# Optimization experiments

Hardware: AMD Instinct MI355X
Metric: run time of the kernel (lower is better)

Reference implementation:

```python
import jax, jax.numpy as jnp
import numpy as np
import math

WS = 8      # window_size
SS = 4      # stride = window_size // 2
NHEADS = 4

def _grid(size, ws, ss):
    n = (size - ws) // ss + 1
    return jnp.arange(n)[:, None] * ss + jnp.arange(ws)[None, :]  # (n, ws)

def _unfold(x, ws, ss):
    # x: (B,C,Hp,Wp) -> (B, L, C, ws*ws), matching torch F.unfold ordering
    B, C, Hp, Wp = x.shape
    ri = _grid(Hp, ws, ss)
    ci = _grid(Wp, ws, ss)
    p = x[:, :, ri][:, :, :, :, ci]  # (B,C,nH,ws,nW,ws)
    nH, nW = ri.shape[0], ci.shape[0]
    p = p.transpose(0, 2, 4, 1, 3, 5).reshape(B, nH * nW, C, ws * ws)
    return p, nH, nW

def _fold(p, Hp, Wp, nH, nW, ws, ss):
    # p: (B, L, C, ws*ws) -> overlap-add to (B,C,Hp,Wp), matching torch F.fold
    B, L, C, _ = p.shape
    p = p.reshape(B, nH, nW, C, ws, ws).transpose(0, 3, 1, 4, 2, 5)  # (B,C,nH,ws,nW,ws)
    rr = _grid(Hp, ws, ss)[:, :, None, None]   # (nH,ws,1,1)
    cc = _grid(Wp, ws, ss)[None, None, :, :]   # (1,1,nW,ws)
    return jnp.zeros((B, C, Hp, Wp), p.dtype).at[:, :, rr, cc].add(p)

def _se(h, w1, w2):
    # squeeze-excite: global avg pool -> 1x1 reduce -> relu -> 1x1 expand -> sigmoid gate
    pooled = h.mean(axis=(2, 3))                                # (B, gc)
    s = jax.nn.sigmoid(jax.nn.relu(pooled @ w1.T) @ w2.T)       # (B, gc)
    return h * s[:, :, None, None]

def _forward(low, high, w_ql, w_kh, w_vh, w_qh, w_kl, w_vl, w_proj_l, w_proj_h,
             se0_w1, se0_w2, se1_w1, se1_w2, se2_w1, se2_w2):
    B, C, H, W = low.shape
    ws, ss = WS, SS
    n_h = 0 if H <= ws else math.ceil((H - ws) / ss)
    n_w = 0 if W <= ws else math.ceil((W - ws) / ss)
    Hp, Wp = n_h * ss + ws, n_w * ss + ws
    pad = ((0, 0), (0, 0), (0, Hp - H), (0, Wp - W))
    low_p = jnp.pad(low, pad)
    high_p = jnp.pad(high, pad)
    base, rem = divmod(C, 3)
    chs = [base + (1 if i < rem else 0) for i in range(3)]
    ofs = np.cumsum([0] + chs)
    sew = [(se0_w1, se0_w2), (se1_w1, se1_w2), (se2_w1, se2_w2)]
    high_dir = jnp.concatenate(
        [_se(high_p[:, ofs[i]:ofs[i + 1]], *sew[i]) for i in range(3)], axis=1)
    lw, nH, nW = _unfold(low_p, ws, ss)    # (B,L,C,Np)
    hw, _, _ = _unfold(high_dir, ws, ss)
    L, Np, d = lw.shape[1], ws * ws, C // NHEADS
    scale = d ** -0.5
    proj = lambda x, w: jnp.einsum('oc,blcn->blon', w, x).reshape(B, L, NHEADS, d, Np)
    a_lh = jax.nn.softmax(jnp.einsum('blhdn,blhdm->blhnm', proj(lw, w_ql), proj(hw, w_kh)) * scale, axis=-1)
    a_hl = jax.nn.softmax(jnp.einsum('blhdn,blhdm->blhnm', proj(hw, w_qh), proj(lw, w_kl)) * scale, axis=-1)
    ol = jnp.einsum('blhnm,blhdm->blhdn', a_lh, proj(hw, w_vh)).reshape(B, L, C, Np)
    oh = jnp.einsum('blhnm,blhdm->blhdn', a_hl, proj(lw, w_vl)).reshape(B, L, C, Np)
    mask = _fold(jnp.ones((1, L, 1, Np), low.dtype), Hp, Wp, nH, nW, ws, ss)  # overlap counts
    out_l = (_fold(ol, Hp, Wp, nH, nW, ws, ss) / mask)[:, :, :H, :W]
    out_h = (_fold(oh, Hp, Wp, nH, nW, ws, ss) / mask)[:, :, :H, :W]
    return (low + jnp.einsum('oc,bchw->bohw', w_proj_l, out_l),
            high + jnp.einsum('oc,bchw->bohw', w_proj_h, out_h))

def setup_inputs() -> dict:
    key = jax.random.key(0)
    ks = jax.random.split(key, 20)
    B, C, H, W = 4, 64, 128, 128
    chs = [22, 21, 21]
    d = {
        'low': jax.random.normal(ks[0], (B, C, H, W), jnp.float32),
        'high': jax.random.normal(ks[1], (B, C, H, W), jnp.float32),
    }
    for i, n in enumerate(['w_ql', 'w_kh', 'w_vh', 'w_qh', 'w_kl', 'w_vl', 'w_proj_l', 'w_proj_h']):
        d[n] = jax.random.normal(ks[2 + i], (C, C), jnp.float32) * (C ** -0.5)
    for i, gc in enumerate(chs):
        d[f'se{i}_w1'] = jax.random.normal(ks[10 + 2 * i], (1, gc), jnp.float32) * 0.1
        d[f'se{i}_w2'] = jax.random.normal(ks[11 + 2 * i], (gc, 1), jnp.float32) * 0.1
    return d

def reference(low, high, w_ql, w_kh, w_vh, w_qh, w_kl, w_vl, w_proj_l, w_proj_h,
              se0_w1, se0_w2, se1_w1, se1_w2, se2_w1, se2_w2):
    return _forward(low, high, w_ql, w_kh, w_vh, w_qh, w_kl, w_vl, w_proj_l, w_proj_h,
                    se0_w1, se0_w2, se1_w1, se1_w2, se2_w1, se2_w2)
```

## Files before the change

### kernel.cpp

```cpp
#include <hip/hip_runtime.h>

typedef short short8 __attribute__((ext_vector_type(8)));
typedef short short4v __attribute__((ext_vector_type(4)));
typedef float f4 __attribute__((ext_vector_type(4)));

#define NB 4
#define NHW 128
#define NPX (NHW*NHW)
#define NWIN 31
#define NL (NWIN*NWIN)
#define SWV(r,c) (((r)<<6) + (((((c)>>3) ^ ((r)&7))<<3) | ((c)&7)))
#define MFMA(a,b,c) __builtin_amdgcn_mfma_f32_16x16x32_bf16(a,b,c,0,0,0)

__device__ __forceinline__ short f2bf(float f) {
    unsigned u = __float_as_uint(f);
    u += 0x7fffu + ((u >> 16) & 1u);
    return (short)(u >> 16);
}
__device__ __forceinline__ float bf2f(short v) {
    return __uint_as_float(((unsigned)(unsigned short)v) << 16);
}

__global__ void k_pool(const float* __restrict__ high, float* __restrict__ pooled) {
    int bc = blockIdx.x;
    const float* src = high + (size_t)bc * NPX;
    float s = 0.f;
    for (int i = threadIdx.x; i < NPX; i += 256) s += src[i];
    for (int off = 32; off > 0; off >>= 1) s += __shfl_down(s, off);
    __shared__ float red[4];
    int lane = threadIdx.x & 63, wv = threadIdx.x >> 6;
    if (lane == 0) red[wv] = s;
    __syncthreads();
    if (threadIdx.x == 0)
        pooled[bc] = (red[0] + red[1] + red[2] + red[3]) * (1.f / NPX);
}

__global__ void k_gate(const float* __restrict__ pooled,
                       const float* __restrict__ w10, const float* __restrict__ w20,
                       const float* __restrict__ w11, const float* __restrict__ w21,
                       const float* __restrict__ w12, const float* __restrict__ w22,
                       float* __restrict__ sgate) {
    __shared__ float pl[256];
    int t = threadIdx.x;
    pl[t] = pooled[t];
    __syncthreads();
    int b = t >> 6, c = t & 63;
    const float* w1; const float* w2; int o0, gc;
    if (c < 22)      { w1 = w10; w2 = w20; o0 = 0;  gc = 22; }
    else if (c < 43) { w1 = w11; w2 = w21; o0 = 22; gc = 21; }
    else             { w1 = w12; w2 = w22; o0 = 43; gc = 21; }
    float a = 0.f;
    for (int k = 0; k < gc; ++k) a += pl[b*64 + o0 + k] * w1[k];
    a = fmaxf(a, 0.f);
    float z = a * w2[c - o0];
    sgate[t] = 1.f / (1.f + __expf(-z));
}

__device__ __forceinline__ void wrange(int x, int& lo, int& hi) {
    lo = (x >= 7) ? ((x - 4) >> 2) : 0;
    hi = x >> 2; if (hi > 30) hi = 30;
}

template<int EMIT>
__global__ __launch_bounds__(256, 6) void k_proj(
    const float* __restrict__ src, const float* __restrict__ gate,
    const float* __restrict__ Wq, const float* __restrict__ Wk, const float* __restrict__ Wv,
    short* __restrict__ Qp, short* __restrict__ Kp, short* __restrict__ Vp) {
    __shared__ __align__(16) short T[8192];
    int b = blockIdx.x >> 7, row = blockIdx.x & 127;
    int t = threadIdx.x;
    const float* sp = src + (size_t)b*64*NPX + row*NHW;
    #pragma unroll
    for (int i = 0; i < 8; ++i) {
        int f = t + i*256;
        int c = f & 63, px = (f >> 6) << 2;
        float4 v = *(const float4*)(sp + (size_t)c*NPX + px);
        float g = gate ? gate[b*64 + c] : 1.f;
        T[SWV(px + 0, c)] = f2bf(v.x * g);
        T[SWV(px + 1, c)] = f2bf(v.y * g);
        T[SWV(px + 2, c)] = f2bf(v.z * g);
        T[SWV(px + 3, c)] = f2bf(v.w * g);
    }
    __syncthreads();
    int w = t >> 6, ln = t & 63, l16 = ln & 15, quad = ln >> 4;
    int orow = 16*w + l16;
    short8 wq[2], wk[2], wv[2];
    #pragma unroll
    for (int kf = 0; kf < 2; ++kf) {
        if (EMIT & 1) {
            const float* p = Wq + orow*64 + kf*32 + quad*8;
            #pragma unroll
            for (int j = 0; j < 8; ++j) wq[kf][j] = f2bf(p[j]);
        }
        if (EMIT & 2) {
            const float* p = Wk + orow*64 + kf*32 + quad*8;
            #pragma unroll
            for (int j = 0; j < 8; ++j) wk[kf][j] = f2bf(p[j]);
        }
        if (EMIT & 4) {
            const float* p = Wv + orow*64 + kf*32 + quad*8;
            #pragma unroll
            for (int j = 0; j < 8; ++j) wv[kf][j] = f2bf(p[j]);
        }
    }
    #pragma unroll
    for (int nt = 0; nt < 8; ++nt) {
        int px = nt*16 + l16;
        short8 xb0 = *(const short8*)(T + SWV(px, quad*8));
        short8 xb1 = *(const short8*)(T + SWV(px, 32 + quad*8));
        size_t clbase = ((size_t)b*NPX + row*NHW + px)*64 + 16*w + quad*4;
        if (EMIT & 1) {
            f4 acc = {0.f,0.f,0.f,0.f};
            acc = MFMA(wq[0], xb0, acc); acc = MFMA(wq[1], xb1, acc);
            short4v sv;
            #pragma unroll
            for (int r = 0; r < 4; ++r) sv[r] = f2bf(acc[r]);
            *(short4v*)(Qp + clbase) = sv;
        }
        if (EMIT & 2) {
            f4 acc = {0.f,0.f,0.f,0.f};
            acc = MFMA(wk[0], xb0, acc); acc = MFMA(wk[1], xb1, acc);
            short4v sv;
            #pragma unroll
            for (int r = 0; r < 4; ++r) sv[r] = f2bf(acc[r]);
            *(short4v*)(Kp + clbase) = sv;
        }
        if (EMIT & 4) {
            f4 acc = {0.f,0.f,0.f,0.f};
            acc = MFMA(wv[0], xb0, acc); acc = MFMA(wv[1], xb1, acc);
            #pragma unroll
            for (int r = 0; r < 4; ++r)
                Vp[((size_t)(b*64 + 16*w + quad*4 + r))*NPX + row*NHW + px] = f2bf(acc[r]);
        }
    }
}

template<int SWZ>
__global__ __launch_bounds__(256, 6) void k_attn(
    const short* __restrict__ Q0, const short* __restrict__ K0, const short* __restrict__ V0,
    const short* __restrict__ Q1, const short* __restrict__ K1, const short* __restrict__ V1,
    short* __restrict__ scr, size_t scr_stride, int nb) {
    __shared__ __align__(16) short Pb[4][1024];
    int bidx = blockIdx.x;
    int pass, b, l;
    if (SWZ) {
        int region = bidx & 7;
        pass = region >> 2; b = region & 3; l = bidx >> 3;
    } else {
        int per = nb * NL;
        pass = bidx / per; int rem2 = bidx - pass*per;
        b = rem2 / NL; l = rem2 - b*NL;
    }
    const short* Qp = pass ? Q1 : Q0;
    const short* Kp = pass ? K1 : K0;
    const short* Vp = pass ? V1 : V0;
    short* scrp = scr + (size_t)pass * scr_stride;
    int wr = l / NWIN, wc = l - (l/NWIN)*NWIN;
    int row0 = wr*4, col0 = wc*4;
    int parity = (wr & 1)*2 + (wc & 1);
    int t = threadIdx.x, w = t >> 6, ln = t & 63, l16 = ln & 15, quad = ln >> 4;
    int h = w;
    short* PT = Pb[w];
    short8 z = {0,0,0,0,0,0,0,0};

    short8 kb[4];
    #pragma unroll
    for (int mt = 0; mt < 4; ++mt) {
        int m = mt*16 + l16;
        int px = (row0 + (m >> 3))*NHW + col0 + (m & 7);
        kb[mt] = (quad < 2) ? *(const short8*)(Kp + ((size_t)b*NPX + px)*64 + h*16 + quad*8) : z;
    }
    short8 va0, va1;
    {
        const short* vb = Vp + ((size_t)(b*64 + h*16 + l16))*NPX;
        const short* p0 = vb + (row0 + quad)*NHW + col0;
        const short* p1 = vb + (row0 + 4 + quad)*NHW + col0;
        short4v a = *(const short4v*)p0, bq = *(const short4v*)(p0 + 4);
        short4v c = *(const short4v*)p1, d = *(const short4v*)(p1 + 4);
        #pragma unroll
        for (int j = 0; j < 4; ++j) { va0[j] = a[j]; va0[4+j] = bq[j]; va1[j] = c[j]; va1[4+j] = d[j]; }
    }

    #pragma unroll
    for (int ntl = 0; ntl < 4; ++ntl) {
        int n = ntl*16 + l16;
        int px = (row0 + (n >> 3))*NHW + col0 + (n & 7);
        short8 qa = (quad < 2) ? *(const short8*)(Qp + ((size_t)b*NPX + px)*64 + h*16 + quad*8) : z;
        f4 s[4];
        #pragma unroll
        for (int mt = 0; mt < 4; ++mt) {
            f4 acc = {0.f,0.f,0.f,0.f};
            s[mt] = MFMA(qa, kb[mt], acc);
        }
        f4 sum = {0.f,0.f,0.f,0.f};
        #pragma unroll
        for (int mt = 0; mt < 4; ++mt)
            #pragma unroll
            for (int r = 0; r < 4; ++r) {
                float e = __expf(fminf(s[mt][r]*0.25f, 30.f));
                s[mt][r] = e; sum[r] += e;
            }
        #pragma unroll
        for (int d = 1; d < 16; d <<= 1)
            #pragma unroll
            for (int r = 0; r < 4; ++r) sum[r] += __shfl_xor(sum[r], d);
        #pragma unroll
        for (int r = 0; r < 4; ++r) sum[r] = 1.f / sum[r];
        #pragma unroll
        for (int mt = 0; mt < 4; ++mt)
            #pragma unroll
            for (int r = 0; r < 4; ++r)
                PT[SWV(quad*4 + r, mt*16 + l16)] = f2bf(s[mt][r] * sum[r]);
        f4 o = {0.f,0.f,0.f,0.f};
        o = MFMA(va0, *(const short8*)(PT + SWV(l16, quad*8)), o);
        o = MFMA(va1, *(const short8*)(PT + SWV(l16, 32 + quad*8)), o);
        short4v sv;
        #pragma unroll
        for (int r = 0; r < 4; ++r) sv[r] = f2bf(o[r]);
        *(short4v*)(scrp + (((size_t)(parity*nb + b))*NPX + px)*64 + h*16 + quad*4) = sv;
    }
}

__global__ __launch_bounds__(256, 6) void k_gather(
    const short* __restrict__ scr, size_t scr_stride,
    const float* __restrict__ r0, const float* __restrict__ r1,
    const float* __restrict__ wp0, const float* __restrict__ wp1,
    float* __restrict__ o0, float* __restrict__ o1, int nb) {
    __shared__ __align__(16) short G[8192];
    int bidx = blockIdx.x;
    int per = nb * NHW;
    int pass = bidx / per; int rem2 = bidx - pass*per;
    int b = rem2 >> 7, hh = rem2 & 127;
    const short* scrp = scr + (size_t)pass * scr_stride;
    const float* resid = pass ? r1 : r0;
    const float* wproj = pass ? wp1 : wp0;
    float* outp = pass ? o1 : o0;
    int t = threadIdx.x;
    int p = t >> 1, c0 = (t & 1)*32;
    int rlo, rhi, clo, chi;
    wrange(hh, rlo, rhi); wrange(p, clo, chi);
    float vr[2], vc[2];
    vr[0] = (rhi > rlo || (rlo & 1) == 0) ? 1.f : 0.f;
    vr[1] = (rhi > rlo || (rlo & 1) == 1) ? 1.f : 0.f;
    vc[0] = (chi > clo || (clo & 1) == 0) ? 1.f : 0.f;
    vc[1] = (chi > clo || (clo & 1) == 1) ? 1.f : 0.f;
    float g[32];
    #pragma unroll
    for (int k = 0; k < 32; ++k) g[k] = 0.f;
    #pragma unroll
    for (int par = 0; par < 4; ++par) {
        float wgt = vr[par >> 1] * vc[par & 1];
        const short* srcp = scrp + (((size_t)(par*nb + b))*NPX + hh*NHW + p)*64 + c0;
        #pragma unroll
        for (int k4 = 0; k4 < 4; ++k4) {
            short8 v = *(const short8*)(srcp + k4*8);
            #pragma unroll
            for (int j = 0; j < 8; ++j) g[k4*8 + j] += wgt * bf2f(v[j]);
        }
    }
    float inv = 1.f / ((float)(rhi - rlo + 1) * (float)(chi - clo + 1));
    #pragma unroll
    for (int k4 = 0; k4 < 4; ++k4) {
        short8 v;
        #pragma unroll
        for (int j = 0; j < 8; ++j) v[j] = f2bf(g[k4*8 + j] * inv);
        *(short8*)(G + SWV(p, c0 + k4*8)) = v;
    }
    __syncthreads();
    int w = t >> 6, ln = t & 63, l16 = ln & 15, quad = ln >> 4;
    short8 wa0, wa1;
    {
        const float* p0 = wproj + (16*w + l16)*64 + quad*8;
        #pragma unroll
        for (int j = 0; j < 8; ++j) { wa0[j] = f2bf(p0[j]); wa1[j] = f2bf(p0[32 + j]); }
    }
    #pragma unroll
    for (int pt = 0; pt < 8; ++pt) {
        f4 acc = {0.f,0.f,0.f,0.f};
        acc = MFMA(wa0, *(const short8*)(G + SWV(pt*16 + l16, quad*8)), acc);
        acc = MFMA(wa1, *(const short8*)(G + SWV(pt*16 + l16, 32 + quad*8)), acc);
        #pragma unroll
        for (int r = 0; r < 4; ++r) {
            size_t gi = (((size_t)(b*64 + 16*w + quad*4 + r))*NHW + hh)*NHW + pt*16 + l16;
            outp[gi] = resid[gi] + acc[r];
        }
    }
}

extern "C" void kernel_launch(void* const* d_in, const int* in_sizes, int n_in,
                              void* d_out, int out_size, void* d_ws, size_t ws_size,
                              hipStream_t stream) {
    const float* low  = (const float*)d_in[0];
    const float* high = (const float*)d_in[1];
    const float* w_ql = (const float*)d_in[2];
    const float* w_kh = (const float*)d_in[3];
    const float* w_vh = (const float*)d_in[4];
    const float* w_qh = (const float*)d_in[5];
    const float* w_kl = (const float*)d_in[6];
    const float* w_vl = (const float*)d_in[7];
    const float* w_pl = (const float*)d_in[8];
    const float* w_ph = (const float*)d_in[9];
    float* out = (float*)d_out;
    float* pooled = (float*)d_ws;
    float* sgate  = pooled + 256;
    short* base = (short*)((char*)d_ws + 2048);
    const size_t PL = (size_t)NB * NPX * 64;
    const size_t plane_f = (size_t)NB * 64 * NPX;
    const size_t SCR = 4 * PL;
    size_t need_fused  = 2048 + (6*PL + 2*SCR) * sizeof(short);
    size_t need_serial = 2048 + (6*PL + SCR) * sizeof(short);
    size_t scr_elems_per_b = 4 * (size_t)NPX * 64;

    k_pool<<<dim3(NB*64), dim3(256), 0, stream>>>(high, pooled);
    k_gate<<<dim3(1), dim3(256), 0, stream>>>(pooled,
        (const float*)d_in[10], (const float*)d_in[11],
        (const float*)d_in[12], (const float*)d_in[13],
        (const float*)d_in[14], (const float*)d_in[15], sgate);

    if (ws_size >= need_serial) {
        short* QL = base;        short* KL = base + PL;   short* VL = base + 2*PL;
        short* QH = base + 3*PL; short* KH = base + 4*PL; short* VH = base + 5*PL;
        short* scr = base + 6*PL;
        k_proj<7><<<dim3(NB*NHW), dim3(256), 0, stream>>>(low,  nullptr, w_ql, w_kl, w_vl, QL, KL, VL);
        k_proj<7><<<dim3(NB*NHW), dim3(256), 0, stream>>>(high, sgate,   w_qh, w_kh, w_vh, QH, KH, VH);
        if (ws_size >= need_fused) {
            k_attn<1><<<dim3(8*NL), dim3(256), 0, stream>>>(QL, KH, VH, QH, KL, VL, scr, SCR, NB);
            k_gather<<<dim3(2*NB*NHW), dim3(256), 0, stream>>>(scr, SCR, low, high,
                w_pl, w_ph, out, out + plane_f, NB);
        } else {
            k_attn<0><<<dim3(NB*NL), dim3(256), 0, stream>>>(QL, KH, VH, nullptr, nullptr, nullptr, scr, 0, NB);
            k_gather<<<dim3(NB*NHW), dim3(256), 0, stream>>>(scr, 0, low, nullptr,
                w_pl, nullptr, out, nullptr, NB);
            k_attn<0><<<dim3(NB*NL), dim3(256), 0, stream>>>(QH, KL, VL, nullptr, nullptr, nullptr, scr, 0, NB);
            k_gather<<<dim3(NB*NHW), dim3(256), 0, stream>>>(scr, 0, high, nullptr,
                w_ph, nullptr, out + plane_f, nullptr, NB);
        }
    } else {
        short* P0 = base; short* P1 = base + PL; short* P2 = base + 2*PL;
        short* scr = base + 3*PL;
        int nbc = 0;
        for (int n = NB; n >= 1; n >>= 1)
            if (ws_size >= 2048 + (3*PL + n*scr_elems_per_b)*sizeof(short)) { nbc = n; break; }
        if (nbc == 0) nbc = 1;
        for (int pass = 0; pass < 2; ++pass) {
            const float* qsrc = pass ? high : low;
            const float* ksrc = pass ? low  : high;
            const float* qg   = pass ? sgate : nullptr;
            const float* kg   = pass ? nullptr : sgate;
            const float* Wq   = pass ? w_qh : w_ql;
            const float* Wk   = pass ? w_kl : w_kh;
            const float* Wv   = pass ? w_vl : w_vh;
            const float* Wp   = pass ? w_ph : w_pl;
            const float* resid = pass ? high : low;
            float* op = out + (size_t)pass * plane_f;
            k_proj<1><<<dim3(NB*NHW), dim3(256), 0, stream>>>(qsrc, qg, Wq, nullptr, nullptr, P0, nullptr, nullptr);
            k_proj<6><<<dim3(NB*NHW), dim3(256), 0, stream>>>(ksrc, kg, nullptr, Wk, Wv, nullptr, P1, P2);
            for (int b0 = 0; b0 < NB; b0 += nbc) {
                int nb = (NB - b0) < nbc ? (NB - b0) : nbc;
                size_t boff = (size_t)b0 * NPX * 64;
                k_attn<0><<<dim3(nb*NL), dim3(256), 0, stream>>>(P0 + boff, P1 + boff, P2 + boff,
                    nullptr, nullptr, nullptr, scr, 0, nb);
                k_gather<<<dim3(nb*NHW), dim3(256), 0, stream>>>(scr, 0, resid + boff, nullptr,
                    Wp, nullptr, op + boff, nullptr, nb);
            }
        }
    }
}
```

Measured before the change: 246.6 us.

## Merge projection launches, compute softmax denominator via MFMA, split gather blocks

The two projection launches become one kernel that picks low or high source by block region, and the 0.25 score scale is folded into Q at projection time. In attention, the shuffle-based softmax sum is replaced by a ones-vector MFMA over the truncated-bf16 probabilities, with normalisation applied after the PV product. Gather blocks now cover half a row each, with the grid doubled and pass/batch interleaved. The goals are to cut launch overhead, cross-lane reductions and per-block register/LDS use, at the cost of bf16 truncation error in the unnormalised probabilities.

After: 218.3 us. 11.5% less time.

```diff
diff --git a/kernel.cpp b/kernel.cpp
--- a/kernel.cpp
+++ b/kernel.cpp
@@ -16,6 +16,9 @@
     unsigned u = __float_as_uint(f);
     u += 0x7fffu + ((u >> 16) & 1u);
     return (short)(u >> 16);
+}
+__device__ __forceinline__ short f2bft(float f) {
+    return (short)(__float_as_uint(f) >> 16);
 }
 __device__ __forceinline__ float bf2f(short v) {
     return __uint_as_float(((unsigned)(unsigned short)v) << 16);
@@ -62,13 +65,11 @@
 }
 
 template<int EMIT>
-__global__ __launch_bounds__(256, 6) void k_proj(
+__device__ __forceinline__ void proj_body(
     const float* __restrict__ src, const float* __restrict__ gate,
     const float* __restrict__ Wq, const float* __restrict__ Wk, const float* __restrict__ Wv,
-    short* __restrict__ Qp, short* __restrict__ Kp, short* __restrict__ Vp) {
-    __shared__ __align__(16) short T[8192];
-    int b = blockIdx.x >> 7, row = blockIdx.x & 127;
-    int t = threadIdx.x;
+    short* __restrict__ Qp, short* __restrict__ Kp, short* __restrict__ Vp,
+    short* T, int b, int row, int t) {
     const float* sp = src + (size_t)b*64*NPX + row*NHW;
     #pragma unroll
     for (int i = 0; i < 8; ++i) {
@@ -114,7 +115,7 @@
             acc = MFMA(wq[0], xb0, acc); acc = MFMA(wq[1], xb1, acc);
             short4v sv;
             #pragma unroll
-            for (int r = 0; r < 4; ++r) sv[r] = f2bf(acc[r]);
+            for (int r = 0; r < 4; ++r) sv[r] = f2bf(acc[r] * 0.25f);
             *(short4v*)(Qp + clbase) = sv;
         }
         if (EMIT & 2) {
@@ -133,6 +134,31 @@
                 Vp[((size_t)(b*64 + 16*w + quad*4 + r))*NPX + row*NHW + px] = f2bf(acc[r]);
         }
     }
+}
+
+template<int EMIT>
+__global__ __launch_bounds__(256, 6) void k_proj(
+    const float* __restrict__ src, const float* __restrict__ gate,
+    const float* __restrict__ Wq, const float* __restrict__ Wk, const float* __restrict__ Wv,
+    short* __restrict__ Qp, short* __restrict__ Kp, short* __restrict__ Vp) {
+    __shared__ __align__(16) short T[8192];
+    proj_body<EMIT>(src, gate, Wq, Wk, Wv, Qp, Kp, Vp, T,
+                    blockIdx.x >> 7, blockIdx.x & 127, threadIdx.x);
+}
+
+__global__ __launch_bounds__(256, 6) void k_proj2(
+    const float* __restrict__ s0, const float* __restrict__ s1, const float* __restrict__ gate,
+    const float* __restrict__ Wq0, const float* __restrict__ Wk0, const float* __restrict__ Wv0,
+    const float* __restrict__ Wq1, const float* __restrict__ Wk1, const float* __restrict__ Wv1,
+    short* __restrict__ Q0, short* __restrict__ K0, short* __restrict__ V0,
+    short* __restrict__ Q1, short* __restrict__ K1, short* __restrict__ V1) {
+    __shared__ __align__(16) short T[8192];
+    int region = blockIdx.x & 7;
+    int ss = region >> 2, b = region & 3, row = blockIdx.x >> 3;
+    if (ss == 0)
+        proj_body<7>(s0, nullptr, Wq0, Wk0, Wv0, Q0, K0, V0, T, b, row, threadIdx.x);
+    else
+        proj_body<7>(s1, gate, Wq1, Wk1, Wv1, Q1, K1, V1, T, b, row, threadIdx.x);
 }
 
 template<int SWZ>
@@ -162,6 +188,8 @@
     int h = w;
     short* PT = Pb[w];
     short8 z = {0,0,0,0,0,0,0,0};
+    const short one = (short)0x3F80;
+    short8 ones = {one,one,one,one,one,one,one,one};
 
     short8 kb[4];
     #pragma unroll
@@ -192,51 +220,52 @@
             f4 acc = {0.f,0.f,0.f,0.f};
             s[mt] = MFMA(qa, kb[mt], acc);
         }
-        f4 sum = {0.f,0.f,0.f,0.f};
         #pragma unroll
         for (int mt = 0; mt < 4; ++mt)
             #pragma unroll
-            for (int r = 0; r < 4; ++r) {
-                float e = __expf(fminf(s[mt][r]*0.25f, 30.f));
-                s[mt][r] = e; sum[r] += e;
-            }
-        #pragma unroll
-        for (int d = 1; d < 16; d <<= 1)
-            #pragma unroll
-            for (int r = 0; r < 4; ++r) sum[r] += __shfl_xor(sum[r], d);
-        #pragma unroll
-        for (int r = 0; r < 4; ++r) sum[r] = 1.f / sum[r];
-        #pragma unroll
-        for (int mt = 0; mt < 4; ++mt)
-            #pragma unroll
             for (int r = 0; r < 4; ++r)
-                PT[SWV(quad*4 + r, mt*16 + l16)] = f2bf(s[mt][r] * sum[r]);
+                PT[SWV(quad*4 + r, mt*16 + l16)] = f2bft(__expf(fminf(s[mt][r], 30.f)));
+        short8 pb0 = *(const short8*)(PT + SWV(l16, quad*8));
+        short8 pb1 = *(const short8*)(PT + SWV(l16, 32 + quad*8));
         f4 o = {0.f,0.f,0.f,0.f};
-        o = MFMA(va0, *(const short8*)(PT + SWV(l16, quad*8)), o);
-        o = MFMA(va1, *(const short8*)(PT + SWV(l16, 32 + quad*8)), o);
+        o = MFMA(va0, pb0, o);
+        o = MFMA(va1, pb1, o);
+        f4 dn = {0.f,0.f,0.f,0.f};
+        dn = MFMA(ones, pb0, dn);
+        dn = MFMA(ones, pb1, dn);
+        float inv = __builtin_amdgcn_rcpf(dn[0]);
         short4v sv;
         #pragma unroll
-        for (int r = 0; r < 4; ++r) sv[r] = f2bf(o[r]);
+        for (int r = 0; r < 4; ++r) sv[r] = f2bf(o[r] * inv);
         *(short4v*)(scrp + (((size_t)(parity*nb + b))*NPX + px)*64 + h*16 + quad*4) = sv;
     }
 }
 
+template<int SWZ>
 __global__ __launch_bounds__(256, 6) void k_gather(
     const short* __restrict__ scr, size_t scr_stride,
     const float* __restrict__ r0, const float* __restrict__ r1,
     const float* __restrict__ wp0, const float* __restrict__ wp1,
     float* __restrict__ o0, float* __restrict__ o1, int nb) {
-    __shared__ __align__(16) short G[8192];
+    __shared__ __align__(16) short G[4096];
     int bidx = blockIdx.x;
-    int per = nb * NHW;
-    int pass = bidx / per; int rem2 = bidx - pass*per;
-    int b = rem2 >> 7, hh = rem2 & 127;
+    int pass, b, hh, half;
+    if (SWZ) {
+        int region = bidx & 7;
+        pass = region >> 2; b = region & 3;
+        int rem2 = bidx >> 3; hh = rem2 >> 1; half = rem2 & 1;
+    } else {
+        pass = 0;
+        b = bidx / (NHW*2); int rem2 = bidx - b*(NHW*2);
+        hh = rem2 >> 1; half = rem2 & 1;
+    }
     const short* scrp = scr + (size_t)pass * scr_stride;
     const float* resid = pass ? r1 : r0;
     const float* wproj = pass ? wp1 : wp0;
     float* outp = pass ? o1 : o0;
     int t = threadIdx.x;
-    int p = t >> 1, c0 = (t & 1)*32;
+    int ploc = t >> 2, c0 = (t & 3)*16;
+    int p = half*64 + ploc;
     int rlo, rhi, clo, chi;
     wrange(hh, rlo, rhi); wrange(p, clo, chi);
     float vr[2], vc[2];
@@ -244,27 +273,27 @@
     vr[1] = (rhi > rlo || (rlo & 1) == 1) ? 1.f : 0.f;
     vc[0] = (chi > clo || (clo & 1) == 0) ? 1.f : 0.f;
     vc[1] = (chi > clo || (clo & 1) == 1) ? 1.f : 0.f;
-    float g[32];
-    #pragma unroll
-    for (int k = 0; k < 32; ++k) g[k] = 0.f;
+    float g[16];
+    #pragma unroll
+    for (int k = 0; k < 16; ++k) g[k] = 0.f;
     #pragma unroll
     for (int par = 0; par < 4; ++par) {
         float wgt = vr[par >> 1] * vc[par & 1];
         const short* srcp = scrp + (((size_t)(par*nb + b))*NPX + hh*NHW + p)*64 + c0;
         #pragma unroll
-        for (int k4 = 0; k4 < 4; ++k4) {
-            short8 v = *(const short8*)(srcp + k4*8);
-            #pragma unroll
-            for (int j = 0; j < 8; ++j) g[k4*8 + j] += wgt * bf2f(v[j]);
+        for (int k8 = 0; k8 < 2; ++k8) {
+            short8 v = *(const short8*)(srcp + k8*8);
+            #pragma unroll
+            for (int j = 0; j < 8; ++j) g[k8*8 + j] += wgt * bf2f(v[j]);
         }
     }
     float inv = 1.f / ((float)(rhi - rlo + 1) * (float)(chi - clo + 1));
     #pragma unroll
-    for (int k4 = 0; k4 < 4; ++k4) {
+    for (int k8 = 0; k8 < 2; ++k8) {
         short8 v;
         #pragma unroll
-        for (int j = 0; j < 8; ++j) v[j] = f2bf(g[k4*8 + j] * inv);
-        *(short8*)(G + SWV(p, c0 + k4*8)) = v;
+        for (int j = 0; j < 8; ++j) v[j] = f2bf(g[k8*8 + j] * inv);
+        *(short8*)(G + SWV(ploc, c0 + k8*8)) = v;
     }
     __syncthreads();
     int w = t >> 6, ln = t & 63, l16 = ln & 15, quad = ln >> 4;
@@ -275,13 +304,13 @@
         for (int j = 0; j < 8; ++j) { wa0[j] = f2bf(p0[j]); wa1[j] = f2bf(p0[32 + j]); }
     }
     #pragma unroll
-    for (int pt = 0; pt < 8; ++pt) {
+    for (int pt = 0; pt < 4; ++pt) {
         f4 acc = {0.f,0.f,0.f,0.f};
         acc = MFMA(wa0, *(const short8*)(G + SWV(pt*16 + l16, quad*8)), acc);
         acc = MFMA(wa1, *(const short8*)(G + SWV(pt*16 + l16, 32 + quad*8)), acc);
         #pragma unroll
         for (int r = 0; r < 4; ++r) {
-            size_t gi = (((size_t)(b*64 + 16*w + quad*4 + r))*NHW + hh)*NHW + pt*16 + l16;
+            size_t gi = (((size_t)(b*64 + 16*w + quad*4 + r))*NHW + hh)*NHW + half*64 + pt*16 + l16;
             outp[gi] = resid[gi] + acc[r];
         }
     }
@@ -321,18 +350,19 @@
         short* QL = base;        short* KL = base + PL;   short* VL = base + 2*PL;
         short* QH = base + 3*PL; short* KH = base + 4*PL; short* VH = base + 5*PL;
         short* scr = base + 6*PL;
-        k_proj<7><<<dim3(NB*NHW), dim3(256), 0, stream>>>(low,  nullptr, w_ql, w_kl, w_vl, QL, KL, VL);
-        k_proj<7><<<dim3(NB*NHW), dim3(256), 0, stream>>>(high, sgate,   w_qh, w_kh, w_vh, QH, KH, VH);
+        k_proj2<<<dim3(8*NHW), dim3(256), 0, stream>>>(low, high, sgate,
+            w_ql, w_kl, w_vl, w_qh, w_kh, w_vh,
+            QL, KL, VL, QH, KH, VH);
         if (ws_size >= need_fused) {
             k_attn<1><<<dim3(8*NL), dim3(256), 0, stream>>>(QL, KH, VH, QH, KL, VL, scr, SCR, NB);
-            k_gather<<<dim3(2*NB*NHW), dim3(256), 0, stream>>>(scr, SCR, low, high,
+            k_gather<1><<<dim3(8*NHW*2), dim3(256), 0, stream>>>(scr, SCR, low, high,
                 w_pl, w_ph, out, out + plane_f, NB);
         } else {
             k_attn<0><<<dim3(NB*NL), dim3(256), 0, stream>>>(QL, KH, VH, nullptr, nullptr, nullptr, scr, 0, NB);
-            k_gather<<<dim3(NB*NHW), dim3(256), 0, stream>>>(scr, 0, low, nullptr,
+            k_gather<0><<<dim3(NB*NHW*2), dim3(256), 0, stream>>>(scr, 0, low, nullptr,
                 w_pl, nullptr, out, nullptr, NB);
             k_attn<0><<<dim3(NB*NL), dim3(256), 0, stream>>>(QH, KL, VL, nullptr, nullptr, nullptr, scr, 0, NB);
-            k_gather<<<dim3(NB*NHW), dim3(256), 0, stream>>>(scr, 0, high, nullptr,
+            k_gather<0><<<dim3(NB*NHW*2), dim3(256), 0, stream>>>(scr, 0, high, nullptr,
                 w_ph, nullptr, out + plane_f, nullptr, NB);
         }
     } else {
@@ -360,7 +390,7 @@
                 size_t boff = (size_t)b0 * NPX * 64;
                 k_attn<0><<<dim3(nb*NL), dim3(256), 0, stream>>>(P0 + boff, P1 + boff, P2 + boff,
                     nullptr, nullptr, nullptr, scr, 0, nb);
-                k_gather<<<dim3(nb*NHW), dim3(256), 0, stream>>>(scr, 0, resid + boff, nullptr,
+                k_gather<0><<<dim3(nb*NHW*2), dim3(256), 0, stream>>>(scr, 0, resid + boff, nullptr,
                     Wp, nullptr, op + boff, nullptr, nb);
             }
         }
```
